# Kernel tuning notes

Hardware: AMD Instinct MI355X
Metric: run time of the kernel (lower is better)

Reference implementation:

```python
import jax, jax.numpy as jnp
import numpy as np

B_SI = 4.1491   # neutron scattering length Si (fm)
B_O = 5.803     # neutron scattering length O (fm)
CUTOFF = 3.5    # tetrahedral neighbour cutoff (A)
BIG = 1e6       # masked-distance sentinel (finite to keep grads NaN-free)


def setup_inputs() -> dict:
    key = jax.random.key(0)
    k1, k2 = jax.random.split(key)
    N, L = 4096, 40.0
    positions = jax.random.uniform(k1, (N, 3), dtype=jnp.float32) * L
    cell = (L * jnp.eye(3)).astype(jnp.float32)
    r_bins = (0.05 + 0.05 * jnp.arange(200, dtype=jnp.float32))      # 0.05..10.0 A
    q_bins = jnp.linspace(0.5, 25.0, 500, dtype=jnp.float32)          # A^-1
    species = jax.random.randint(k2, (N,), 0, 3, dtype=jnp.int32)     # 0=Si, 1/2=O
    return {"positions": positions, "cell": cell, "r_bins": r_bins,
            "q_bins": q_bins, "species": species}


def _pair_geometry(positions, cell):
    # Minimum-image displacements under a general periodic cell.
    disp = positions[:, None, :] - positions[None, :, :]        # [N,N,3]
    frac = disp @ jnp.linalg.inv(cell)
    frac = frac - jnp.round(frac)
    disp = frac @ cell
    d2 = jnp.sum(disp * disp, axis=-1)                           # [N,N]
    self_mask = jnp.eye(positions.shape[0], dtype=bool)
    dist = jnp.sqrt(jnp.where(self_mask, 1.0, d2))               # safe sqrt on diag
    return disp, dist, self_mask


def reference(positions, cell, r_bins, q_bins, species):
    N = positions.shape[0]
    nbins = r_bins.shape[0]
    dtype = positions.dtype

    disp, dist, self_mask = _pair_geometry(positions, cell)

    # --- neutron-weighted G(r): differentiable linear (cloud-in-cell) binning ---
    b = jnp.where(species == 0, B_SI, B_O).astype(dtype)         # per-atom scattering length
    w = (b[:, None] * b[None, :]) / (jnp.mean(b) ** 2)           # Faber-Ziman pair weights
    r0, dr = r_bins[0], r_bins[1] - r_bins[0]
    x = (dist - r0) / dr
    i0 = jnp.floor(x).astype(jnp.int32)
    f = x - i0.astype(dtype)
    valid = (~self_mask) & (i0 >= 0) & (i0 < nbins - 1)
    w0 = jnp.where(valid, w * (1.0 - f), 0.0).ravel()
    w1 = jnp.where(valid, w * f, 0.0).ravel()
    i0f = jnp.clip(i0, 0, nbins - 1).ravel()
    hist = (jnp.zeros(nbins, dtype)
            .at[i0f].add(w0)
            .at[jnp.clip(i0f + 1, 0, nbins - 1)].add(w1))
    V = jnp.abs(jnp.linalg.det(cell))
    rho = N / V
    shell = 4.0 * jnp.pi * r_bins ** 2 * dr                       # ideal-gas shell volume
    G_r = hist / (N * rho * shell)                                # [nbins]

    # --- total correlation function T(r) = 4 pi rho r G(r) ---
    T_r = 4.0 * jnp.pi * rho * r_bins * G_r

    # --- structure factor S(Q) = 1 + 4 pi rho int r^2 (G(r)-1) sinc(Qr) dr ---
    qr = q_bins[:, None] * r_bins[None, :]                        # [nQ, nr]
    integrand = (r_bins ** 2) * (G_r - 1.0)
    S_Q = 1.0 + 4.0 * jnp.pi * rho * dr * jnp.sum(
        integrand[None, :] * jnp.sinc(qr / jnp.pi), axis=1)

    # --- tetrahedral order parameter q_tet over Si centres with O neighbours ---
    central = species == 0
    nbr_ok = (species != 0)[None, :] & (~self_mask)
    nd = jnp.where(nbr_ok, dist, BIG)
    negd, idx = jax.lax.top_k(-nd, 4)                             # 4 nearest O per atom
    d4 = -negd                                                    # [N,4]
    u = jnp.take_along_axis(disp, idx[:, :, None], axis=1) / d4[:, :, None]  # unit vecs
    cosang = jnp.einsum('nkd,nld->nkl', u, u)                     # [N,4,4]
    pair_mask = jnp.triu(jnp.ones((4, 4), bool), 1)               # 6 angle pairs
    q_i = 1.0 - (3.0 / 8.0) * jnp.sum(((cosang + 1.0 / 3.0) ** 2) * pair_mask, axis=(1, 2))
    vf = (central & (d4[:, 3] < CUTOFF)).astype(dtype)            # needs 4 nbrs in cutoff
    q_tet = jnp.sum(q_i * vf) / jnp.maximum(jnp.sum(vf), 1.0)

    return G_r, T_r, S_Q, q_tet
```

## Files before the change

### kernel.cpp

```cpp
#include <hip/hip_runtime.h>
#include <climits>
#include <math.h>


#define B_SI_F 4.1491f
#define B_O_F  5.803f
#define CUTOFF_F 3.5f
#define NCOPIES 16

#define WS_HIST 16
#define WS_QV   4096

__device__ __forceinline__ bool dless(float da, int ia, float db, int ib) {
    return (da < db) || (da == db && ia < ib);
}

struct CellK {
    float ci0, ci1, ci2, ci3, ci4, ci5, ci6, ci7, ci8;
    float c0, c1, c2, c3, c4, c5, c6, c7, c8;
};

__device__ __forceinline__ CellK make_cell(const float* __restrict__ cellm,
                                           bool& diag) {
    CellK K;
    K.c0 = cellm[0]; K.c1 = cellm[1]; K.c2 = cellm[2];
    K.c3 = cellm[3]; K.c4 = cellm[4]; K.c5 = cellm[5];
    K.c6 = cellm[6]; K.c7 = cellm[7]; K.c8 = cellm[8];
    double m0 = K.c0, m1 = K.c1, m2 = K.c2;
    double m3 = K.c3, m4 = K.c4, m5 = K.c5;
    double m6 = K.c6, m7 = K.c7, m8 = K.c8;
    double det = m0*(m4*m8 - m5*m7) - m1*(m3*m8 - m5*m6) + m2*(m3*m7 - m4*m6);
    double rd = 1.0 / det;
    K.ci0 = (float)( (m4*m8 - m5*m7) * rd);
    K.ci1 = (float)(-(m1*m8 - m2*m7) * rd);
    K.ci2 = (float)( (m1*m5 - m2*m4) * rd);
    K.ci3 = (float)(-(m3*m8 - m5*m6) * rd);
    K.ci4 = (float)( (m0*m8 - m2*m6) * rd);
    K.ci5 = (float)(-(m0*m5 - m2*m3) * rd);
    K.ci6 = (float)( (m3*m7 - m4*m6) * rd);
    K.ci7 = (float)(-(m0*m7 - m1*m6) * rd);
    K.ci8 = (float)( (m0*m4 - m1*m3) * rd);
    diag = (K.c1 == 0.0f) && (K.c2 == 0.0f) && (K.c3 == 0.0f) &&
           (K.c5 == 0.0f) && (K.c6 == 0.0f) && (K.c7 == 0.0f);
    return K;
}

template<bool DIAG>
__device__ __forceinline__ void min_image(const CellK& K,
                                          float dx, float dy, float dz,
                                          float& ex, float& ey, float& ez) {
    if (DIAG) {
        float t0 = dx * K.ci0, t1 = dy * K.ci4, t2 = dz * K.ci8;
        t0 -= rintf(t0);  t1 -= rintf(t1);  t2 -= rintf(t2);
        ex = t0 * K.c0;  ey = t1 * K.c4;  ez = t2 * K.c8;
    } else {
        float f0 = dx*K.ci0 + dy*K.ci3 + dz*K.ci6;
        float f1 = dx*K.ci1 + dy*K.ci4 + dz*K.ci7;
        float f2 = dx*K.ci2 + dy*K.ci5 + dz*K.ci8;
        f0 -= rintf(f0);  f1 -= rintf(f1);  f2 -= rintf(f2);
        ex = f0*K.c0 + f1*K.c3 + f2*K.c6;
        ey = f0*K.c1 + f1*K.c4 + f2*K.c7;
        ez = f0*K.c2 + f1*K.c5 + f2*K.c8;
    }
}

template<bool DIAG>
__device__ __forceinline__ void hist_sweep(const CellK& K,
                                           const float4* __restrict__ sj,
                                           int lbase,
                                           float xi, float yi, float zi, float wi,
                                           float rb0, float inv_dr, int nbins_m1,
                                           float* shist) {
    #pragma unroll 4
    for (int l = 0; l < 32; ++l) {
        const float4 pj = sj[lbase + l];
        float ex, ey, ez;
        min_image<DIAG>(K, xi - pj.x, yi - pj.y, zi - pj.z, ex, ey, ez);
        float dist = __builtin_amdgcn_sqrtf(fmaf(ex, ex, fmaf(ey, ey, ez * ez)));
        float x  = (dist - rb0) * inv_dr;
        float fl = floorf(x);
        int   i0 = (int)fl;
        if (i0 >= 0 && i0 < nbins_m1) {
            float w = wi * pj.w;
            float f = x - fl;
            atomicAdd(&shist[i0],     w * (1.0f - f));
            atomicAdd(&shist[i0 + 1], w * f);
        }
    }
}

template<bool DIAG>
__device__ __forceinline__ void top4_sweep_s(const CellK& K,
                                             const float* __restrict__ pos,
                                             const int* __restrict__ species,
                                             int N, int lane,
                                             float xi, float yi, float zi,
                                             float& e0, float& e1, float& e2, float& e3,
                                             int& j0, int& j1, int& j2, int& j3) {
    #pragma unroll 4
    for (int k = lane; k < N; k += 64) {
        int   sp = species[k];
        float px = pos[3*k], py = pos[3*k+1], pz = pos[3*k+2];
        float ex, ey, ez;
        min_image<DIAG>(K, xi - px, yi - py, zi - pz, ex, ey, ez);
        float d2 = fmaf(ex, ex, fmaf(ey, ey, ez * ez));
        float c  = (sp != 0) ? d2 : 1e30f;
        int   jc = k;
        if (dless(c, jc, e3, j3)) {
            bool lt2 = dless(c, jc, e2, j2);
            bool lt1 = dless(c, jc, e1, j1);
            bool lt0 = dless(c, jc, e0, j0);
            e3 = lt2 ? e2 : c;               j3 = lt2 ? j2 : jc;
            e2 = lt2 ? (lt1 ? e1 : c) : e2;  j2 = lt2 ? (lt1 ? j1 : jc) : j2;
            e1 = lt1 ? (lt0 ? e0 : c) : e1;  j1 = lt1 ? (lt0 ? j0 : jc) : j1;
            e0 = lt0 ? c : e0;               j0 = lt0 ? jc : j0;
        }
    }
}

__global__ __launch_bounds__(256) void k_main(const float* __restrict__ cellm,
                                              const float* __restrict__ pos,
                                              const int* __restrict__ species,
                                              const float* __restrict__ rbins,
                                              float* __restrict__ ws,
                                              int N, int nbins, int T, int P2) {
    const int tid = threadIdx.x;
    const int bid = blockIdx.x;

    bool diag;
    const CellK K = make_cell(cellm, diag);

    if (bid < P2) {
        __shared__ float shist[256];
        __shared__ float sjf[64 * 4];
        shist[tid] = 0.0f;

        const int jhalf = bid & 1;
        int rem = bid >> 1;
        int ti = 0;
        while (rem >= T - ti) { rem -= T - ti; ti++; }
        const int tj = ti + rem;
        const int jb0 = tj * 128 + jhalf * 64;

        if (tid < 192) {
            int g = 3 * jb0 + tid;
            float v = (g < 3 * N) ? pos[g] : 0.0f;
            sjf[(tid / 3) * 4 + (tid % 3)] = v;
        } else {
            int a = tid - 192;
            int ja = jb0 + a;
            float b = (ja < N) ? ((species[ja] == 0) ? B_SI_F : B_O_F) : 0.0f;
            sjf[a * 4 + 3] = b;
        }

        const float rb0     = rbins[0];
        const float inv_dr  = 1.0f / (rbins[1] - rbins[0]);
        const int   nbins_m1 = nbins - 1;

        const int il  = tid & 127;
        const int sub = tid >> 7;
        const int i   = ti * 128 + il;
        const int ig  = min(i, N - 1);
        const float xi = pos[3*ig], yi = pos[3*ig+1], zi = pos[3*ig+2];
        const float b_i = (species[ig] == 0) ? B_SI_F : B_O_F;
        const float wmul = (ti == tj) ? 1.0f : 2.0f;
        const float wi = (i < N) ? b_i * wmul : 0.0f;

        __syncthreads();

        const float4* sj = (const float4*)sjf;
        if (diag) hist_sweep<true >(K, sj, sub * 32, xi, yi, zi, wi, rb0, inv_dr, nbins_m1, shist);
        else      hist_sweep<false>(K, sj, sub * 32, xi, yi, zi, wi, rb0, inv_dr, nbins_m1, shist);

        __syncthreads();

        float* gh = ws + WS_HIST + (size_t)(bid % NCOPIES) * nbins;
        for (int t = tid; t < nbins; t += 256) {
            float h = shist[t];
            if (h != 0.0f) atomicAdd(&gh[t], h);
        }
        return;
    }

    const int s = __builtin_amdgcn_readfirstlane((bid - P2) * 4 + (tid >> 6));
    if (s >= N) return;
    const int lane = tid & 63;
    float* __restrict__ qv = ws + WS_QV;

    if (species[s] != 0) {
        if (lane == 0) { qv[2*s] = 0.0f; qv[2*s + 1] = 0.0f; }
        return;
    }

    const float xi = pos[3*s], yi = pos[3*s+1], zi = pos[3*s+2];

    float e0 = 1e30f, e1 = 1e30f, e2 = 1e30f, e3 = 1e30f;
    int   j0 = INT_MAX, j1 = INT_MAX, j2 = INT_MAX, j3 = INT_MAX;

    if (diag) top4_sweep_s<true >(K, pos, species, N, lane, xi, yi, zi, e0, e1, e2, e3, j0, j1, j2, j3);
    else      top4_sweep_s<false>(K, pos, species, N, lane, xi, yi, zi, e0, e1, e2, e3, j0, j1, j2, j3);

    float r0d, r1d, r2d, r3d;  int r0j, r1j, r2j, r3j;
    #define EXTRACT_MIN(RD, RJ)                                        \
    {                                                                  \
        float md = e0; int mj = j0;                                    \
        for (int off = 32; off > 0; off >>= 1) {                       \
            float od = __shfl_xor(md, off, 64);                        \
            int   oj = __shfl_xor(mj, off, 64);                        \
            bool keep = dless(md, mj, od, oj);                         \
            md = keep ? md : od;                                       \
            mj = keep ? mj : oj;                                       \
        }                                                              \
        RD = md; RJ = mj;                                              \
        bool pop = (j0 == mj);                                         \
        e0 = pop ? e1 : e0;  j0 = pop ? j1 : j0;                       \
        e1 = pop ? e2 : e1;  j1 = pop ? j2 : j1;                       \
        e2 = pop ? e3 : e2;  j2 = pop ? j3 : j2;                       \
        e3 = pop ? 1e30f : e3;  j3 = pop ? INT_MAX : j3;               \
    }
    EXTRACT_MIN(r0d, r0j)
    EXTRACT_MIN(r1d, r1j)
    EXTRACT_MIN(r2d, r2j)
    EXTRACT_MIN(r3d, r3j)
    #undef EXTRACT_MIN

    if (lane == 0) {
        float qiv = 0.0f, vf = 0.0f;
        float dd0 = sqrtf(r0d), dd1 = sqrtf(r1d), dd2 = sqrtf(r2d), dd3 = sqrtf(r3d);
        if (dd3 < CUTOFF_F) {
            float ux[4], uy[4], uz[4];
            float dd[4]  = {dd0, dd1, dd2, dd3};
            int   jj4[4] = {r0j, r1j, r2j, r3j};
            #pragma unroll
            for (int k = 0; k < 4; ++k) {
                int jk = jj4[k];
                float ex, ey, ez;
                if (diag) min_image<true >(K, xi - pos[3*jk], yi - pos[3*jk+1], zi - pos[3*jk+2], ex, ey, ez);
                else      min_image<false>(K, xi - pos[3*jk], yi - pos[3*jk+1], zi - pos[3*jk+2], ex, ey, ez);
                ux[k] = ex / dd[k];
                uy[k] = ey / dd[k];
                uz[k] = ez / dd[k];
            }
            float s2 = 0.0f;
            #pragma unroll
            for (int k = 0; k < 4; ++k)
                #pragma unroll
                for (int l = k + 1; l < 4; ++l) {
                    float cs = ux[k]*ux[l] + uy[k]*uy[l] + uz[k]*uz[l];
                    float t  = cs + (1.0f / 3.0f);
                    s2 += t * t;
                }
            qiv = 1.0f - 0.375f * s2;
            vf  = 1.0f;
        }
        qv[2*s]     = qiv;
        qv[2*s + 1] = vf;
    }
}

__device__ __forceinline__ float fast_sinc(float x) {
    float rev = x * 0.15915494309189535f;
    rev -= rintf(rev);
    float sn = __builtin_amdgcn_sinf(rev);
    return sn * __builtin_amdgcn_rcpf(x);
}

__global__ __launch_bounds__(256) void k_finalize(const float* __restrict__ cellm,
                                                  const float* __restrict__ ws,
                                                  const float* __restrict__ rbins,
                                                  const float* __restrict__ qbins,
                                                  const int* __restrict__ species,
                                                  float* __restrict__ out,
                                                  int N, int nbins, int nq) {
    __shared__ float2 srw[256];
    __shared__ float rq[256], rv[256];
    __shared__ int   scnt[256];
    const int tid = threadIdx.x;

    double m0 = cellm[0], m1 = cellm[1], m2 = cellm[2];
    double m3 = cellm[3], m4 = cellm[4], m5 = cellm[5];
    double m6 = cellm[6], m7 = cellm[7], m8 = cellm[8];
    double det = m0*(m4*m8 - m5*m7) - m1*(m3*m8 - m5*m6) + m2*(m3*m7 - m4*m6);
    const float rho = (float)((double)N / fabs(det));

    {
        int c = 0;
        for (int k = tid; k < N; k += 256) c += (species[k] == 0) ? 1 : 0;
        scnt[tid] = c;
    }
    __syncthreads();
    for (int s = 128; s > 0; s >>= 1) {
        if (tid < s) scnt[tid] += scnt[tid + s];
        __syncthreads();
    }
    const int nSi = scnt[0];
    const float mean_b  = ((float)nSi * B_SI_F + (float)(N - nSi) * B_O_F) / (float)N;
    const float w_scale = 1.0f / (mean_b * mean_b);

    const float dr  = rbins[1] - rbins[0];
    const float FOURPI = 4.0f * 3.14159265358979323846f;

    for (int t = tid; t < nbins; t += blockDim.x) {
        float h = 0.0f;
        #pragma unroll
        for (int c = 0; c < NCOPIES; ++c) h += ws[WS_HIST + c * nbins + t];
        h *= w_scale;
        float r = rbins[t];
        float shell = FOURPI * r * r * dr;
        float g = h / ((float)N * rho * shell);
        srw[t] = make_float2(r, r * r * (g - 1.0f));
        if (blockIdx.x == 0) {
            out[t] = g;
            out[nbins + t] = FOURPI * rho * r * g;
        }
    }

    if (blockIdx.x == 0) {
        const float* qv = ws + WS_QV;
        float sq = 0.0f, sv = 0.0f;
        for (int s = tid; s < N; s += 256) {
            sq += qv[2*s];
            sv += qv[2*s + 1];
        }
        rq[tid] = sq; rv[tid] = sv;
    }
    __syncthreads();
    if (blockIdx.x == 0) {
        for (int s = 128; s > 0; s >>= 1) {
            if (tid < s) { rq[tid] += rq[tid + s]; rv[tid] += rv[tid + s]; }
            __syncthreads();
        }
        if (tid == 0)
            out[2 * nbins + nq] = rq[0] / fmaxf(rv[0], 1.0f);
    }

    int q = blockIdx.x * blockDim.x + tid;
    if (q < nq) {
        float qq = qbins[q];
        float s0 = 0.0f, s1 = 0.0f, s2 = 0.0f, s3 = 0.0f;
        int t = 0;
        for (; t + 4 <= nbins; t += 4) {
            float2 a = srw[t], b = srw[t+1], c = srw[t+2], d = srw[t+3];
            s0 += a.y * fast_sinc(qq * a.x);
            s1 += b.y * fast_sinc(qq * b.x);
            s2 += c.y * fast_sinc(qq * c.x);
            s3 += d.y * fast_sinc(qq * d.x);
        }
        for (; t < nbins; ++t) {
            float2 a = srw[t];
            s0 += a.y * fast_sinc(qq * a.x);
        }
        float s = (s0 + s1) + (s2 + s3);
        out[2 * nbins + q] = 1.0f + FOURPI * rho * dr * s;
    }
}

extern "C" void kernel_launch(void* const* d_in, const int* in_sizes, int n_in,
                              void* d_out, int out_size, void* d_ws, size_t ws_size,
                              hipStream_t stream) {
    const float* pos     = (const float*)d_in[0];
    const float* cell    = (const float*)d_in[1];
    const float* rbins   = (const float*)d_in[2];
    const float* qbins   = (const float*)d_in[3];
    const int*   species = (const int*)d_in[4];
    float* out = (float*)d_out;
    float* ws  = (float*)d_ws;

    const int N     = in_sizes[4];
    const int nbins = in_sizes[2];
    const int nq    = in_sizes[3];

    const int T  = (N + 127) / 128;
    const int P2 = T * (T + 1);
    const int BT = (N + 3) / 4;

    k_main<<<P2 + BT, 256, 0, stream>>>(cell, pos, species, rbins, ws, N, nbins, T, P2);
    k_finalize<<<(nq + 255) / 256, 256, 0, stream>>>(cell, ws, rbins, qbins, species, out, N, nbins, nq);
}
```

Before: 108.8 us.

## Collect cutoff-neighbour candidates during histogram pass instead of brute-force top-4 scan

The separate per-Si brute-force nearest-four-oxygen scan over all N atoms is removed. While binning distances, the histogram kernel records Si–O pairs within a slightly padded cutoff into per-atom candidate lists using global atomic counters, with capacity 32. A single extra finalize block then picks the top-4 from each candidate list and falls back to a full scan if a list overflows. This eliminates about a thousand scan blocks. In exchange it adds global atomics to the hot histogram loop and a serial single-block tail, and it relies on the counter workspace starting at zero.

```diff
diff --git a/kernel.cpp b/kernel.cpp
--- a/kernel.cpp
+++ b/kernel.cpp
@@ -6,10 +6,12 @@
 #define B_SI_F 4.1491f
 #define B_O_F  5.803f
 #define CUTOFF_F 3.5f
+#define CUT_SLACK 3.5005f
 #define NCOPIES 16
+#define CAP 32
 
 #define WS_HIST 16
-#define WS_QV   4096
+#define WS_CNT  4096
 
 __device__ __forceinline__ bool dless(float da, int ia, float db, int ib) {
     return (da < db) || (da == db && ia < ib);
@@ -67,10 +69,13 @@
 template<bool DIAG>
 __device__ __forceinline__ void hist_sweep(const CellK& K,
                                            const float4* __restrict__ sj,
-                                           int lbase,
+                                           int lbase, int jb0,
                                            float xi, float yi, float zi, float wi,
                                            float rb0, float inv_dr, int nbins_m1,
-                                           float* shist) {
+                                           float* shist,
+                                           bool iSi, bool iO, bool offdiag, int iidx,
+                                           float* __restrict__ cnt,
+                                           int* __restrict__ cand) {
     #pragma unroll 4
     for (int l = 0; l < 32; ++l) {
         const float4 pj = sj[lbase + l];
@@ -86,34 +91,18 @@
             atomicAdd(&shist[i0],     w * (1.0f - f));
             atomicAdd(&shist[i0 + 1], w * f);
         }
-    }
-}
-
-template<bool DIAG>
-__device__ __forceinline__ void top4_sweep_s(const CellK& K,
-                                             const float* __restrict__ pos,
-                                             const int* __restrict__ species,
-                                             int N, int lane,
-                                             float xi, float yi, float zi,
-                                             float& e0, float& e1, float& e2, float& e3,
-                                             int& j0, int& j1, int& j2, int& j3) {
-    #pragma unroll 4
-    for (int k = lane; k < N; k += 64) {
-        int   sp = species[k];
-        float px = pos[3*k], py = pos[3*k+1], pz = pos[3*k+2];
-        float ex, ey, ez;
-        min_image<DIAG>(K, xi - px, yi - py, zi - pz, ex, ey, ez);
-        float d2 = fmaf(ex, ex, fmaf(ey, ey, ez * ez));
-        float c  = (sp != 0) ? d2 : 1e30f;
-        int   jc = k;
-        if (dless(c, jc, e3, j3)) {
-            bool lt2 = dless(c, jc, e2, j2);
-            bool lt1 = dless(c, jc, e1, j1);
-            bool lt0 = dless(c, jc, e0, j0);
-            e3 = lt2 ? e2 : c;               j3 = lt2 ? j2 : jc;
-            e2 = lt2 ? (lt1 ? e1 : c) : e2;  j2 = lt2 ? (lt1 ? j1 : jc) : j2;
-            e1 = lt1 ? (lt0 ? e0 : c) : e1;  j1 = lt1 ? (lt0 ? j0 : jc) : j1;
-            e0 = lt0 ? c : e0;               j0 = lt0 ? jc : j0;
+        if (dist < CUT_SLACK) {
+            const int jg = jb0 + lbase + l;
+            if (iSi && pj.w == B_O_F) {
+                float old = atomicAdd(&cnt[iidx], 1.0f);
+                int slot = (int)rintf(old);
+                if (slot < CAP) cand[iidx * CAP + slot] = jg;
+            }
+            if (offdiag && iO && pj.w == B_SI_F) {
+                float old = atomicAdd(&cnt[jg], 1.0f);
+                int slot = (int)rintf(old);
+                if (slot < CAP) cand[jg * CAP + slot] = iidx;
+            }
         }
     }
 }
@@ -123,138 +112,146 @@
                                               const int* __restrict__ species,
                                               const float* __restrict__ rbins,
                                               float* __restrict__ ws,
-                                              int N, int nbins, int T, int P2) {
+                                              int N, int nbins, int T) {
     const int tid = threadIdx.x;
     const int bid = blockIdx.x;
 
     bool diag;
     const CellK K = make_cell(cellm, diag);
 
-    if (bid < P2) {
-        __shared__ float shist[256];
-        __shared__ float sjf[64 * 4];
-        shist[tid] = 0.0f;
-
-        const int jhalf = bid & 1;
-        int rem = bid >> 1;
-        int ti = 0;
-        while (rem >= T - ti) { rem -= T - ti; ti++; }
-        const int tj = ti + rem;
-        const int jb0 = tj * 128 + jhalf * 64;
-
-        if (tid < 192) {
-            int g = 3 * jb0 + tid;
-            float v = (g < 3 * N) ? pos[g] : 0.0f;
-            sjf[(tid / 3) * 4 + (tid % 3)] = v;
+    __shared__ float shist[256];
+    __shared__ float sjf[64 * 4];
+    shist[tid] = 0.0f;
+
+    const int jhalf = bid & 1;
+    int rem = bid >> 1;
+    int ti = 0;
+    while (rem >= T - ti) { rem -= T - ti; ti++; }
+    const int tj = ti + rem;
+    const int jb0 = tj * 128 + jhalf * 64;
+
+    if (tid < 192) {
+        int g = 3 * jb0 + tid;
+        float v = (g < 3 * N) ? pos[g] : 0.0f;
+        sjf[(tid / 3) * 4 + (tid % 3)] = v;
+    } else {
+        int a = tid - 192;
+        int ja = jb0 + a;
+        float b = (ja < N) ? ((species[ja] == 0) ? B_SI_F : B_O_F) : 0.0f;
+        sjf[a * 4 + 3] = b;
+    }
+
+    const float rb0     = rbins[0];
+    const float inv_dr  = 1.0f / (rbins[1] - rbins[0]);
+    const int   nbins_m1 = nbins - 1;
+
+    const int il  = tid & 127;
+    const int sub = tid >> 7;
+    const int i   = ti * 128 + il;
+    const int ig  = min(i, N - 1);
+    const float xi = pos[3*ig], yi = pos[3*ig+1], zi = pos[3*ig+2];
+    const int   spi = species[ig];
+    const float b_i = (spi == 0) ? B_SI_F : B_O_F;
+    const float wmul = (ti == tj) ? 1.0f : 2.0f;
+    const float wi = (i < N) ? b_i * wmul : 0.0f;
+    const bool iSi = (i < N) && (spi == 0);
+    const bool iO  = (i < N) && (spi != 0);
+    const bool offdiag = (ti != tj);
+
+    float* cnt  = ws + WS_CNT;
+    int*   cand = (int*)(ws + WS_CNT + N);
+
+    __syncthreads();
+
+    const float4* sj = (const float4*)sjf;
+    if (diag) hist_sweep<true >(K, sj, sub * 32, jb0, xi, yi, zi, wi, rb0, inv_dr, nbins_m1, shist, iSi, iO, offdiag, i, cnt, cand);
+    else      hist_sweep<false>(K, sj, sub * 32, jb0, xi, yi, zi, wi, rb0, inv_dr, nbins_m1, shist, iSi, iO, offdiag, i, cnt, cand);
+
+    __syncthreads();
+
+    float* gh = ws + WS_HIST + (size_t)(bid % NCOPIES) * nbins;
+    for (int t = tid; t < nbins; t += 256) {
+        float h = shist[t];
+        if (h != 0.0f) atomicAdd(&gh[t], h);
+    }
+}
+
+__device__ __forceinline__ void ins4(float c, int jc,
+                                     float& e0, float& e1, float& e2, float& e3,
+                                     int& j0, int& j1, int& j2, int& j3) {
+    if (dless(c, jc, e3, j3)) {
+        bool lt2 = dless(c, jc, e2, j2);
+        bool lt1 = dless(c, jc, e1, j1);
+        bool lt0 = dless(c, jc, e0, j0);
+        e3 = lt2 ? e2 : c;               j3 = lt2 ? j2 : jc;
+        e2 = lt2 ? (lt1 ? e1 : c) : e2;  j2 = lt2 ? (lt1 ? j1 : jc) : j2;
+        e1 = lt1 ? (lt0 ? e0 : c) : e1;  j1 = lt1 ? (lt0 ? j0 : jc) : j1;
+        e0 = lt0 ? c : e0;               j0 = lt0 ? jc : j0;
+    }
+}
+
+template<bool DIAG>
+__device__ __forceinline__ void tet_compute(const CellK& K,
+                                            const float* __restrict__ pos,
+                                            const int* __restrict__ species,
+                                            const float* __restrict__ cnt,
+                                            const int* __restrict__ cand,
+                                            int N, int tid,
+                                            float& sq, float& sv) {
+    for (int s = tid; s < N; s += 256) {
+        if (species[s] != 0) continue;
+        const float xi = pos[3*s], yi = pos[3*s+1], zi = pos[3*s+2];
+        const int c = (int)rintf(cnt[s]);
+
+        float e0 = 1e30f, e1 = 1e30f, e2 = 1e30f, e3 = 1e30f;
+        int   j0 = INT_MAX, j1 = INT_MAX, j2 = INT_MAX, j3 = INT_MAX;
+
+        if (c <= CAP) {
+            for (int k = 0; k < c; ++k) {
+                int j = cand[s * CAP + k];
+                float ex, ey, ez;
+                min_image<DIAG>(K, xi - pos[3*j], yi - pos[3*j+1], zi - pos[3*j+2], ex, ey, ez);
+                float d2 = fmaf(ex, ex, fmaf(ey, ey, ez * ez));
+                ins4(d2, j, e0, e1, e2, e3, j0, j1, j2, j3);
+            }
         } else {
-            int a = tid - 192;
-            int ja = jb0 + a;
-            float b = (ja < N) ? ((species[ja] == 0) ? B_SI_F : B_O_F) : 0.0f;
-            sjf[a * 4 + 3] = b;
-        }
-
-        const float rb0     = rbins[0];
-        const float inv_dr  = 1.0f / (rbins[1] - rbins[0]);
-        const int   nbins_m1 = nbins - 1;
-
-        const int il  = tid & 127;
-        const int sub = tid >> 7;
-        const int i   = ti * 128 + il;
-        const int ig  = min(i, N - 1);
-        const float xi = pos[3*ig], yi = pos[3*ig+1], zi = pos[3*ig+2];
-        const float b_i = (species[ig] == 0) ? B_SI_F : B_O_F;
-        const float wmul = (ti == tj) ? 1.0f : 2.0f;
-        const float wi = (i < N) ? b_i * wmul : 0.0f;
-
-        __syncthreads();
-
-        const float4* sj = (const float4*)sjf;
-        if (diag) hist_sweep<true >(K, sj, sub * 32, xi, yi, zi, wi, rb0, inv_dr, nbins_m1, shist);
-        else      hist_sweep<false>(K, sj, sub * 32, xi, yi, zi, wi, rb0, inv_dr, nbins_m1, shist);
-
-        __syncthreads();
-
-        float* gh = ws + WS_HIST + (size_t)(bid % NCOPIES) * nbins;
-        for (int t = tid; t < nbins; t += 256) {
-            float h = shist[t];
-            if (h != 0.0f) atomicAdd(&gh[t], h);
-        }
-        return;
-    }
-
-    const int s = __builtin_amdgcn_readfirstlane((bid - P2) * 4 + (tid >> 6));
-    if (s >= N) return;
-    const int lane = tid & 63;
-    float* __restrict__ qv = ws + WS_QV;
-
-    if (species[s] != 0) {
-        if (lane == 0) { qv[2*s] = 0.0f; qv[2*s + 1] = 0.0f; }
-        return;
-    }
-
-    const float xi = pos[3*s], yi = pos[3*s+1], zi = pos[3*s+2];
-
-    float e0 = 1e30f, e1 = 1e30f, e2 = 1e30f, e3 = 1e30f;
-    int   j0 = INT_MAX, j1 = INT_MAX, j2 = INT_MAX, j3 = INT_MAX;
-
-    if (diag) top4_sweep_s<true >(K, pos, species, N, lane, xi, yi, zi, e0, e1, e2, e3, j0, j1, j2, j3);
-    else      top4_sweep_s<false>(K, pos, species, N, lane, xi, yi, zi, e0, e1, e2, e3, j0, j1, j2, j3);
-
-    float r0d, r1d, r2d, r3d;  int r0j, r1j, r2j, r3j;
-    #define EXTRACT_MIN(RD, RJ)                                        \
-    {                                                                  \
-        float md = e0; int mj = j0;                                    \
-        for (int off = 32; off > 0; off >>= 1) {                       \
-            float od = __shfl_xor(md, off, 64);                        \
-            int   oj = __shfl_xor(mj, off, 64);                        \
-            bool keep = dless(md, mj, od, oj);                         \
-            md = keep ? md : od;                                       \
-            mj = keep ? mj : oj;                                       \
-        }                                                              \
-        RD = md; RJ = mj;                                              \
-        bool pop = (j0 == mj);                                         \
-        e0 = pop ? e1 : e0;  j0 = pop ? j1 : j0;                       \
-        e1 = pop ? e2 : e1;  j1 = pop ? j2 : j1;                       \
-        e2 = pop ? e3 : e2;  j2 = pop ? j3 : j2;                       \
-        e3 = pop ? 1e30f : e3;  j3 = pop ? INT_MAX : j3;               \
-    }
-    EXTRACT_MIN(r0d, r0j)
-    EXTRACT_MIN(r1d, r1j)
-    EXTRACT_MIN(r2d, r2j)
-    EXTRACT_MIN(r3d, r3j)
-    #undef EXTRACT_MIN
-
-    if (lane == 0) {
-        float qiv = 0.0f, vf = 0.0f;
-        float dd0 = sqrtf(r0d), dd1 = sqrtf(r1d), dd2 = sqrtf(r2d), dd3 = sqrtf(r3d);
-        if (dd3 < CUTOFF_F) {
-            float ux[4], uy[4], uz[4];
-            float dd[4]  = {dd0, dd1, dd2, dd3};
-            int   jj4[4] = {r0j, r1j, r2j, r3j};
-            #pragma unroll
-            for (int k = 0; k < 4; ++k) {
-                int jk = jj4[k];
+            for (int j = 0; j < N; ++j) {
+                if (j == s || species[j] == 0) continue;
                 float ex, ey, ez;
-                if (diag) min_image<true >(K, xi - pos[3*jk], yi - pos[3*jk+1], zi - pos[3*jk+2], ex, ey, ez);
-                else      min_image<false>(K, xi - pos[3*jk], yi - pos[3*jk+1], zi - pos[3*jk+2], ex, ey, ez);
-                ux[k] = ex / dd[k];
-                uy[k] = ey / dd[k];
-                uz[k] = ez / dd[k];
-            }
-            float s2 = 0.0f;
-            #pragma unroll
-            for (int k = 0; k < 4; ++k)
+                min_image<DIAG>(K, xi - pos[3*j], yi - pos[3*j+1], zi - pos[3*j+2], ex, ey, ez);
+                float d2 = fmaf(ex, ex, fmaf(ey, ey, ez * ez));
+                ins4(d2, j, e0, e1, e2, e3, j0, j1, j2, j3);
+            }
+        }
+
+        if (j3 != INT_MAX) {
+            float dd0 = sqrtf(e0), dd1 = sqrtf(e1), dd2 = sqrtf(e2), dd3 = sqrtf(e3);
+            if (dd3 < CUTOFF_F) {
+                float ux[4], uy[4], uz[4];
+                float dd[4]  = {dd0, dd1, dd2, dd3};
+                int   jj4[4] = {j0, j1, j2, j3};
                 #pragma unroll
-                for (int l = k + 1; l < 4; ++l) {
-                    float cs = ux[k]*ux[l] + uy[k]*uy[l] + uz[k]*uz[l];
-                    float t  = cs + (1.0f / 3.0f);
-                    s2 += t * t;
+                for (int k = 0; k < 4; ++k) {
+                    int jk = jj4[k];
+                    float ex, ey, ez;
+                    min_image<DIAG>(K, xi - pos[3*jk], yi - pos[3*jk+1], zi - pos[3*jk+2], ex, ey, ez);
+                    ux[k] = ex / dd[k];
+                    uy[k] = ey / dd[k];
+                    uz[k] = ez / dd[k];
                 }
-            qiv = 1.0f - 0.375f * s2;
-            vf  = 1.0f;
-        }
-        qv[2*s]     = qiv;
-        qv[2*s + 1] = vf;
+                float s2 = 0.0f;
+                #pragma unroll
+                for (int k = 0; k < 4; ++k)
+                    #pragma unroll
+                    for (int l = k + 1; l < 4; ++l) {
+                        float cs = ux[k]*ux[l] + uy[k]*uy[l] + uz[k]*uz[l];
+                        float t  = cs + (1.0f / 3.0f);
+                        s2 += t * t;
+                    }
+                sq += 1.0f - 0.375f * s2;
+                sv += 1.0f;
+            }
+        }
     }
 }
 
@@ -270,12 +267,32 @@
                                                   const float* __restrict__ rbins,
                                                   const float* __restrict__ qbins,
                                                   const int* __restrict__ species,
+                                                  const float* __restrict__ pos,
                                                   float* __restrict__ out,
                                                   int N, int nbins, int nq) {
     __shared__ float2 srw[256];
     __shared__ float rq[256], rv[256];
     __shared__ int   scnt[256];
     const int tid = threadIdx.x;
+
+    if (blockIdx.x == gridDim.x - 1) {
+        bool diag;
+        const CellK K = make_cell(cellm, diag);
+        const float* cnt  = ws + WS_CNT;
+        const int*   cand = (const int*)(ws + WS_CNT + N);
+        float sq = 0.0f, sv = 0.0f;
+        if (diag) tet_compute<true >(K, pos, species, cnt, cand, N, tid, sq, sv);
+        else      tet_compute<false>(K, pos, species, cnt, cand, N, tid, sq, sv);
+        rq[tid] = sq; rv[tid] = sv;
+        __syncthreads();
+        for (int s = 128; s > 0; s >>= 1) {
+            if (tid < s) { rq[tid] += rq[tid + s]; rv[tid] += rv[tid + s]; }
+            __syncthreads();
+        }
+        if (tid == 0)
+            out[2 * nbins + nq] = rq[0] / fmaxf(rv[0], 1.0f);
+        return;
+    }
 
     double m0 = cellm[0], m1 = cellm[1], m2 = cellm[2];
     double m3 = cellm[3], m4 = cellm[4], m5 = cellm[5];
@@ -314,25 +331,7 @@
             out[nbins + t] = FOURPI * rho * r * g;
         }
     }
-
-    if (blockIdx.x == 0) {
-        const float* qv = ws + WS_QV;
-        float sq = 0.0f, sv = 0.0f;
-        for (int s = tid; s < N; s += 256) {
-            sq += qv[2*s];
-            sv += qv[2*s + 1];
-        }
-        rq[tid] = sq; rv[tid] = sv;
-    }
     __syncthreads();
-    if (blockIdx.x == 0) {
-        for (int s = 128; s > 0; s >>= 1) {
-            if (tid < s) { rq[tid] += rq[tid + s]; rv[tid] += rv[tid + s]; }
-            __syncthreads();
-        }
-        if (tid == 0)
-            out[2 * nbins + nq] = rq[0] / fmaxf(rv[0], 1.0f);
-    }
 
     int q = blockIdx.x * blockDim.x + tid;
     if (q < nq) {
@@ -372,8 +371,8 @@
 
     const int T  = (N + 127) / 128;
     const int P2 = T * (T + 1);
-    const int BT = (N + 3) / 4;
-
-    k_main<<<P2 + BT, 256, 0, stream>>>(cell, pos, species, rbins, ws, N, nbins, T, P2);
-    k_finalize<<<(nq + 255) / 256, 256, 0, stream>>>(cell, ws, rbins, qbins, species, out, N, nbins, nq);
-}
+    const int QB = (nq + 255) / 256;
+
+    k_main<<<P2, 256, 0, stream>>>(cell, pos, species, rbins, ws, N, nbins, T);
+    k_finalize<<<QB + 1, 256, 0, stream>>>(cell, ws, rbins, qbins, species, pos, out, N, nbins, nq);
+}
```

Result: slower. 185.6 us (+70.5%).

## Collect Si-O neighbour candidates during histogram sweep to skip full top-4 scans

Applied to the files above, without the earlier changes.

During the pair-histogram sweep, each Si atom now records the O atoms within a slightly padded cutoff into a per-atom candidate list, with counts kept by atomics. A separate tetrahedral kernel then picks the four nearest from at most 32 candidates instead of scanning all N atoms. It falls back to the full scan when the list overflows and resets the counters for the next call. This adds global atomics in the hot histogram loop and an extra kernel launch. It also makes the tetrahedral step depend on the histogram kernel finishing first.

```diff
diff --git a/kernel.cpp b/kernel.cpp
--- a/kernel.cpp
+++ b/kernel.cpp
@@ -6,10 +6,12 @@
 #define B_SI_F 4.1491f
 #define B_O_F  5.803f
 #define CUTOFF_F 3.5f
+#define CUT_SLACK 3.5005f
 #define NCOPIES 16
+#define CAP 32
 
 #define WS_HIST 16
-#define WS_QV   4096
+#define WS_CNT  4096
 
 __device__ __forceinline__ bool dless(float da, int ia, float db, int ib) {
     return (da < db) || (da == db && ia < ib);
@@ -67,10 +69,13 @@
 template<bool DIAG>
 __device__ __forceinline__ void hist_sweep(const CellK& K,
                                            const float4* __restrict__ sj,
-                                           int lbase,
+                                           int lbase, int jb0,
                                            float xi, float yi, float zi, float wi,
                                            float rb0, float inv_dr, int nbins_m1,
-                                           float* shist) {
+                                           float* shist,
+                                           bool iSi, bool iO, bool offdiag, int iidx,
+                                           float* __restrict__ cnt,
+                                           int* __restrict__ cand) {
     #pragma unroll 4
     for (int l = 0; l < 32; ++l) {
         const float4 pj = sj[lbase + l];
@@ -86,6 +91,88 @@
             atomicAdd(&shist[i0],     w * (1.0f - f));
             atomicAdd(&shist[i0 + 1], w * f);
         }
+        if (dist < CUT_SLACK) {
+            const int jg = jb0 + lbase + l;
+            if (iSi && pj.w == B_O_F) {
+                float old = atomicAdd(&cnt[iidx], 1.0f);
+                int slot = (int)rintf(old);
+                if (slot < CAP) cand[iidx * CAP + slot] = jg;
+            }
+            if (offdiag && iO && pj.w == B_SI_F) {
+                float old = atomicAdd(&cnt[jg], 1.0f);
+                int slot = (int)rintf(old);
+                if (slot < CAP) cand[jg * CAP + slot] = iidx;
+            }
+        }
+    }
+}
+
+__global__ __launch_bounds__(256) void k_main(const float* __restrict__ cellm,
+                                              const float* __restrict__ pos,
+                                              const int* __restrict__ species,
+                                              const float* __restrict__ rbins,
+                                              float* __restrict__ ws,
+                                              int N, int nbins, int T) {
+    const int tid = threadIdx.x;
+    const int bid = blockIdx.x;
+
+    bool diag;
+    const CellK K = make_cell(cellm, diag);
+
+    __shared__ float shist[256];
+    __shared__ float sjf[64 * 4];
+    shist[tid] = 0.0f;
+
+    const int jhalf = bid & 1;
+    int rem = bid >> 1;
+    int ti = 0;
+    while (rem >= T - ti) { rem -= T - ti; ti++; }
+    const int tj = ti + rem;
+    const int jb0 = tj * 128 + jhalf * 64;
+
+    if (tid < 192) {
+        int g = 3 * jb0 + tid;
+        float v = (g < 3 * N) ? pos[g] : 0.0f;
+        sjf[(tid / 3) * 4 + (tid % 3)] = v;
+    } else {
+        int a = tid - 192;
+        int ja = jb0 + a;
+        float b = (ja < N) ? ((species[ja] == 0) ? B_SI_F : B_O_F) : 0.0f;
+        sjf[a * 4 + 3] = b;
+    }
+
+    const float rb0     = rbins[0];
+    const float inv_dr  = 1.0f / (rbins[1] - rbins[0]);
+    const int   nbins_m1 = nbins - 1;
+
+    const int il  = tid & 127;
+    const int sub = tid >> 7;
+    const int i   = ti * 128 + il;
+    const int ig  = min(i, N - 1);
+    const float xi = pos[3*ig], yi = pos[3*ig+1], zi = pos[3*ig+2];
+    const int   spi = species[ig];
+    const float b_i = (spi == 0) ? B_SI_F : B_O_F;
+    const float wmul = (ti == tj) ? 1.0f : 2.0f;
+    const float wi = (i < N) ? b_i * wmul : 0.0f;
+    const bool iSi = (i < N) && (spi == 0);
+    const bool iO  = (i < N) && (spi != 0);
+    const bool offdiag = (ti != tj);
+
+    float* cnt  = ws + WS_CNT;
+    int*   cand = (int*)(ws + WS_CNT + 3 * (size_t)N);
+
+    __syncthreads();
+
+    const float4* sj = (const float4*)sjf;
+    if (diag) hist_sweep<true >(K, sj, sub * 32, jb0, xi, yi, zi, wi, rb0, inv_dr, nbins_m1, shist, iSi, iO, offdiag, i, cnt, cand);
+    else      hist_sweep<false>(K, sj, sub * 32, jb0, xi, yi, zi, wi, rb0, inv_dr, nbins_m1, shist, iSi, iO, offdiag, i, cnt, cand);
+
+    __syncthreads();
+
+    float* gh = ws + WS_HIST + (size_t)(bid % NCOPIES) * nbins;
+    for (int t = tid; t < nbins; t += 256) {
+        float h = shist[t];
+        if (h != 0.0f) atomicAdd(&gh[t], h);
     }
 }
 
@@ -93,18 +180,17 @@
 __device__ __forceinline__ void top4_sweep_s(const CellK& K,
                                              const float* __restrict__ pos,
                                              const int* __restrict__ species,
-                                             int N, int lane,
+                                             int N, int lane, int self,
                                              float xi, float yi, float zi,
                                              float& e0, float& e1, float& e2, float& e3,
                                              int& j0, int& j1, int& j2, int& j3) {
-    #pragma unroll 4
     for (int k = lane; k < N; k += 64) {
         int   sp = species[k];
         float px = pos[3*k], py = pos[3*k+1], pz = pos[3*k+2];
         float ex, ey, ez;
         min_image<DIAG>(K, xi - px, yi - py, zi - pz, ex, ey, ez);
         float d2 = fmaf(ex, ex, fmaf(ey, ey, ez * ez));
-        float c  = (sp != 0) ? d2 : 1e30f;
+        float c  = (sp != 0 && k != self) ? d2 : 1e30f;
         int   jc = k;
         if (dless(c, jc, e3, j3)) {
             bool lt2 = dless(c, jc, e2, j2);
@@ -118,87 +204,46 @@
     }
 }
 
-__global__ __launch_bounds__(256) void k_main(const float* __restrict__ cellm,
-                                              const float* __restrict__ pos,
-                                              const int* __restrict__ species,
-                                              const float* __restrict__ rbins,
-                                              float* __restrict__ ws,
-                                              int N, int nbins, int T, int P2) {
-    const int tid = threadIdx.x;
-    const int bid = blockIdx.x;
-
-    bool diag;
-    const CellK K = make_cell(cellm, diag);
-
-    if (bid < P2) {
-        __shared__ float shist[256];
-        __shared__ float sjf[64 * 4];
-        shist[tid] = 0.0f;
-
-        const int jhalf = bid & 1;
-        int rem = bid >> 1;
-        int ti = 0;
-        while (rem >= T - ti) { rem -= T - ti; ti++; }
-        const int tj = ti + rem;
-        const int jb0 = tj * 128 + jhalf * 64;
-
-        if (tid < 192) {
-            int g = 3 * jb0 + tid;
-            float v = (g < 3 * N) ? pos[g] : 0.0f;
-            sjf[(tid / 3) * 4 + (tid % 3)] = v;
-        } else {
-            int a = tid - 192;
-            int ja = jb0 + a;
-            float b = (ja < N) ? ((species[ja] == 0) ? B_SI_F : B_O_F) : 0.0f;
-            sjf[a * 4 + 3] = b;
-        }
-
-        const float rb0     = rbins[0];
-        const float inv_dr  = 1.0f / (rbins[1] - rbins[0]);
-        const int   nbins_m1 = nbins - 1;
-
-        const int il  = tid & 127;
-        const int sub = tid >> 7;
-        const int i   = ti * 128 + il;
-        const int ig  = min(i, N - 1);
-        const float xi = pos[3*ig], yi = pos[3*ig+1], zi = pos[3*ig+2];
-        const float b_i = (species[ig] == 0) ? B_SI_F : B_O_F;
-        const float wmul = (ti == tj) ? 1.0f : 2.0f;
-        const float wi = (i < N) ? b_i * wmul : 0.0f;
-
-        __syncthreads();
-
-        const float4* sj = (const float4*)sjf;
-        if (diag) hist_sweep<true >(K, sj, sub * 32, xi, yi, zi, wi, rb0, inv_dr, nbins_m1, shist);
-        else      hist_sweep<false>(K, sj, sub * 32, xi, yi, zi, wi, rb0, inv_dr, nbins_m1, shist);
-
-        __syncthreads();
-
-        float* gh = ws + WS_HIST + (size_t)(bid % NCOPIES) * nbins;
-        for (int t = tid; t < nbins; t += 256) {
-            float h = shist[t];
-            if (h != 0.0f) atomicAdd(&gh[t], h);
-        }
-        return;
-    }
-
-    const int s = __builtin_amdgcn_readfirstlane((bid - P2) * 4 + (tid >> 6));
+__global__ __launch_bounds__(256) void k_tet(const float* __restrict__ cellm,
+                                             const float* __restrict__ pos,
+                                             const int* __restrict__ species,
+                                             float* __restrict__ ws, int N) {
+    const int s = __builtin_amdgcn_readfirstlane(blockIdx.x * 4 + (threadIdx.x >> 6));
     if (s >= N) return;
-    const int lane = tid & 63;
-    float* __restrict__ qv = ws + WS_QV;
+    const int lane = threadIdx.x & 63;
+
+    float* cnt = ws + WS_CNT;
+    float* qv  = ws + WS_CNT + N;
+    const int* cand = (const int*)(ws + WS_CNT + 3 * (size_t)N);
 
     if (species[s] != 0) {
         if (lane == 0) { qv[2*s] = 0.0f; qv[2*s + 1] = 0.0f; }
         return;
     }
 
+    bool diag;
+    const CellK K = make_cell(cellm, diag);
     const float xi = pos[3*s], yi = pos[3*s+1], zi = pos[3*s+2];
+
+    const int c = (int)rintf(cnt[s]);
+    if (lane == 0) cnt[s] = 0.0f;
 
     float e0 = 1e30f, e1 = 1e30f, e2 = 1e30f, e3 = 1e30f;
     int   j0 = INT_MAX, j1 = INT_MAX, j2 = INT_MAX, j3 = INT_MAX;
 
-    if (diag) top4_sweep_s<true >(K, pos, species, N, lane, xi, yi, zi, e0, e1, e2, e3, j0, j1, j2, j3);
-    else      top4_sweep_s<false>(K, pos, species, N, lane, xi, yi, zi, e0, e1, e2, e3, j0, j1, j2, j3);
+    if (c <= CAP) {
+        if (lane < c) {
+            int j = cand[s * CAP + lane];
+            float ex, ey, ez;
+            if (diag) min_image<true >(K, xi - pos[3*j], yi - pos[3*j+1], zi - pos[3*j+2], ex, ey, ez);
+            else      min_image<false>(K, xi - pos[3*j], yi - pos[3*j+1], zi - pos[3*j+2], ex, ey, ez);
+            e0 = fmaf(ex, ex, fmaf(ey, ey, ez * ez));
+            j0 = j;
+        }
+    } else {
+        if (diag) top4_sweep_s<true >(K, pos, species, N, lane, s, xi, yi, zi, e0, e1, e2, e3, j0, j1, j2, j3);
+        else      top4_sweep_s<false>(K, pos, species, N, lane, s, xi, yi, zi, e0, e1, e2, e3, j0, j1, j2, j3);
+    }
 
     float r0d, r1d, r2d, r3d;  int r0j, r1j, r2j, r3j;
     #define EXTRACT_MIN(RD, RJ)                                        \
@@ -226,32 +271,34 @@
 
     if (lane == 0) {
         float qiv = 0.0f, vf = 0.0f;
-        float dd0 = sqrtf(r0d), dd1 = sqrtf(r1d), dd2 = sqrtf(r2d), dd3 = sqrtf(r3d);
-        if (dd3 < CUTOFF_F) {
-            float ux[4], uy[4], uz[4];
-            float dd[4]  = {dd0, dd1, dd2, dd3};
-            int   jj4[4] = {r0j, r1j, r2j, r3j};
-            #pragma unroll
-            for (int k = 0; k < 4; ++k) {
-                int jk = jj4[k];
-                float ex, ey, ez;
-                if (diag) min_image<true >(K, xi - pos[3*jk], yi - pos[3*jk+1], zi - pos[3*jk+2], ex, ey, ez);
-                else      min_image<false>(K, xi - pos[3*jk], yi - pos[3*jk+1], zi - pos[3*jk+2], ex, ey, ez);
-                ux[k] = ex / dd[k];
-                uy[k] = ey / dd[k];
-                uz[k] = ez / dd[k];
+        if (r3j != INT_MAX) {
+            float dd0 = sqrtf(r0d), dd1 = sqrtf(r1d), dd2 = sqrtf(r2d), dd3 = sqrtf(r3d);
+            if (dd3 < CUTOFF_F) {
+                float ux[4], uy[4], uz[4];
+                float dd[4]  = {dd0, dd1, dd2, dd3};
+                int   jj4[4] = {r0j, r1j, r2j, r3j};
+                #pragma unroll
+                for (int k = 0; k < 4; ++k) {
+                    int jk = jj4[k];
+                    float ex, ey, ez;
+                    if (diag) min_image<true >(K, xi - pos[3*jk], yi - pos[3*jk+1], zi - pos[3*jk+2], ex, ey, ez);
+                    else      min_image<false>(K, xi - pos[3*jk], yi - pos[3*jk+1], zi - pos[3*jk+2], ex, ey, ez);
+                    ux[k] = ex / dd[k];
+                    uy[k] = ey / dd[k];
+                    uz[k] = ez / dd[k];
+                }
+                float s2 = 0.0f;
+                #pragma unroll
+                for (int k = 0; k < 4; ++k)
+                    #pragma unroll
+                    for (int l = k + 1; l < 4; ++l) {
+                        float cs = ux[k]*ux[l] + uy[k]*uy[l] + uz[k]*uz[l];
+                        float t  = cs + (1.0f / 3.0f);
+                        s2 += t * t;
+                    }
+                qiv = 1.0f - 0.375f * s2;
+                vf  = 1.0f;
             }
-            float s2 = 0.0f;
-            #pragma unroll
-            for (int k = 0; k < 4; ++k)
-                #pragma unroll
-                for (int l = k + 1; l < 4; ++l) {
-                    float cs = ux[k]*ux[l] + uy[k]*uy[l] + uz[k]*uz[l];
-                    float t  = cs + (1.0f / 3.0f);
-                    s2 += t * t;
-                }
-            qiv = 1.0f - 0.375f * s2;
-            vf  = 1.0f;
         }
         qv[2*s]     = qiv;
         qv[2*s + 1] = vf;
@@ -316,7 +363,7 @@
     }
 
     if (blockIdx.x == 0) {
-        const float* qv = ws + WS_QV;
+        const float* qv = ws + WS_CNT + N;
         float sq = 0.0f, sv = 0.0f;
         for (int s = tid; s < N; s += 256) {
             sq += qv[2*s];
@@ -373,7 +420,9 @@
     const int T  = (N + 127) / 128;
     const int P2 = T * (T + 1);
     const int BT = (N + 3) / 4;
-
-    k_main<<<P2 + BT, 256, 0, stream>>>(cell, pos, species, rbins, ws, N, nbins, T, P2);
-    k_finalize<<<(nq + 255) / 256, 256, 0, stream>>>(cell, ws, rbins, qbins, species, out, N, nbins, nq);
-}
+    const int QB = (nq + 255) / 256;
+
+    k_main<<<P2, 256, 0, stream>>>(cell, pos, species, rbins, ws, N, nbins, T);
+    k_tet<<<BT, 256, 0, stream>>>(cell, pos, species, ws, N);
+    k_finalize<<<QB, 256, 0, stream>>>(cell, ws, rbins, qbins, species, out, N, nbins, nq);
+}
```

After: 96.84 us. 11.0% less time.
